# Optimization experiments

Hardware: AMD Instinct MI355X
Metric: run time of the kernel (lower is better)

The kernel has to match this reference:

```python
import jax, jax.numpy as jnp
import numpy as np

B, S, H, HD = 8, 1024, 16, 64
D = H * HD
NINF = -10000.0
EPS = 1e-6


def setup_inputs() -> dict:
    key = jax.random.key(0)
    ks = jax.random.split(key, 6)
    std = 0.02
    return {
        "x": jax.random.normal(ks[0], (B, S, D), jnp.float32),
        "mask": jax.random.randint(ks[1], (B, S), 0, 2, jnp.int32),
        "wq": jax.random.normal(ks[2], (D, D), jnp.float32) * std,
        "bq": jnp.zeros((D,), jnp.float32),
        "wk": jax.random.normal(ks[3], (D, D), jnp.float32) * std,
        "bk": jnp.zeros((D,), jnp.float32),
        "wv": jax.random.normal(ks[4], (D, D), jnp.float32) * std,
        "bv": jnp.zeros((D,), jnp.float32),
        "wo": jax.random.normal(ks[5], (D, D), jnp.float32) * std,
        "bo": jnp.zeros((D,), jnp.float32),
        "gamma": jnp.ones((D,), jnp.float32),
        "beta": jnp.zeros((D,), jnp.float32),
    }


def _heads(t):
    # [B,S,D] -> [B,H,S,HD]
    return t.reshape(t.shape[0], t.shape[1], H, HD).transpose(0, 2, 1, 3)


def _layernorm(x, gamma, beta):
    mu = jnp.mean(x, -1, keepdims=True)
    var = jnp.mean(jnp.square(x - mu), -1, keepdims=True)
    return (x - mu) * jax.lax.rsqrt(var + EPS) * gamma + beta


def reference(x, mask, wq, bq, wk, bk, wv, bv, wo, bo, gamma, beta):
    q = _heads(x @ wq + bq)
    k = _heads(x @ wk + bk)
    v = _heads(x @ wv + bv)
    scores = jnp.einsum("bhqd,bhkd->bhqk", q, k) / np.sqrt(HD).astype(np.float32)
    # padding mask broadcast over key axis: 1 = masked
    scores = scores + mask.astype(jnp.float32)[:, None, None, :] * NINF
    attn = jax.nn.softmax(scores, axis=-1)
    ctx = jnp.einsum("bhqk,bhkd->bhqd", attn, v)  # [B,H,S,HD]
    ctx = ctx.transpose(0, 2, 1, 3).reshape(B, S, D)
    out = _layernorm(x + ctx @ wo + bo, gamma, beta)
    return out
```

## Files before the change

kernel.cpp:

```cpp
#include <hip/hip_runtime.h>
#include <stdint.h>

typedef unsigned short u16;
typedef unsigned int u32;
typedef __bf16 b16x8 __attribute__((ext_vector_type(8)));
typedef float f32x4 __attribute__((ext_vector_type(4)));

#define B_ 8
#define S_ 1024
#define H_ 16
#define HD_ 64
#define D_ 1024
#define M_ 8192

__device__ __forceinline__ u16 f2bf(float f) {
  u32 u = __float_as_uint(f);
  return (u16)((u + 0x7fffu + ((u >> 16) & 1u)) >> 16);
}
__device__ __forceinline__ u16 bfbits(float f) {
  union {
    __bf16 b;
    u16 u;
  } c;
  c.b = (__bf16)f;
  return c.u;
}

__device__ __forceinline__ f32x4 mfma16(b16x8 a, b16x8 b, f32x4 c) {
  return __builtin_amdgcn_mfma_f32_16x16x32_bf16(a, b, c, 0, 0, 0);
}

__device__ __forceinline__ void cp16(const u16* g, u16* l) {
  __builtin_amdgcn_global_load_lds(
      (const __attribute__((address_space(1))) u32*)(g),
      (__attribute__((address_space(3))) u32*)(l), 16, 0, 0);
}

__global__ __launch_bounds__(1024) void wconv_kernel(
    const float* __restrict__ w0, const float* __restrict__ w1,
    const float* __restrict__ w2, const float* __restrict__ w3,
    u16* __restrict__ t0, u16* __restrict__ t1, u16* __restrict__ t2,
    u16* __restrict__ t3) {
  __shared__ float tile[32][33];
  const int z = blockIdx.z;
  const float* src = (z == 0) ? w0 : (z == 1) ? w1 : (z == 2) ? w2 : w3;
  u16* dst = (z == 0) ? t0 : (z == 1) ? t1 : (z == 2) ? t2 : t3;
  const int tx = threadIdx.x, ty = threadIdx.y;
  const int x0 = blockIdx.x * 32, y0 = blockIdx.y * 32;
  tile[ty][tx] = src[(size_t)(y0 + ty) * D_ + x0 + tx];
  __syncthreads();
  dst[(size_t)(x0 + ty) * D_ + y0 + tx] = f2bf(tile[tx][ty]);
}

__global__ __launch_bounds__(256) void xconv_kernel(const float* __restrict__ x,
                                                    u16* __restrict__ xb) {
  const size_t i = ((size_t)blockIdx.x * 256 + threadIdx.x) * 4;
  const float4 v = *(const float4*)(x + i);
  u16 o[4] = {f2bf(v.x), f2bf(v.y), f2bf(v.z), f2bf(v.w)};
  uint2 pack;
  pack.x = ((u32)o[1] << 16) | o[0];
  pack.y = ((u32)o[3] << 16) | o[2];
  *(uint2*)(xb + i) = pack;
}

#define ABUF_ 16384
#define BBUF_ 8192
#define BUFSZ_ (ABUF_ + BBUF_)

__device__ __forceinline__ void gemm256x128_mainloop(
    const u16* __restrict__ A, const u16* __restrict__ BT, int K, int m0,
    int n0, u16* lds, f32x4 (&acc)[8][2]) {
  const int t = threadIdx.x;
  const int lane = t & 63;
  const int l15 = lane & 15;
  const int q4 = lane >> 4;
  const int w = t >> 6;
  const int wm = w >> 2;
  const int wn = w & 3;

  const f32x4 zero = {0.f, 0.f, 0.f, 0.f};
#pragma unroll
  for (int mt = 0; mt < 8; ++mt)
#pragma unroll
    for (int nt = 0; nt < 2; ++nt) acc[mt][nt] = zero;

  const int rbase = t >> 3;
  const int scol = ((t & 7) ^ (rbase & 7)) * 8;
  const u16* Ag = A + (size_t)(m0 + rbase) * K + scol;
  const u16* Bg = BT + (size_t)(n0 + rbase) * K + scol;
  const int sx = l15 & 7;

  auto STAGE = [&](int kt, int bufi) {
    u16* Ab = lds + bufi * BUFSZ_;
    u16* Bb = Ab + ABUF_;
    const int k0 = kt * 64;
#pragma unroll
    for (int c = 0; c < 4; ++c)
      cp16(Ag + (size_t)(c * 64) * K + k0, Ab + c * 4096 + t * 8);
#pragma unroll
    for (int c = 0; c < 2; ++c)
      cp16(Bg + (size_t)(c * 64) * K + k0, Bb + c * 4096 + t * 8);
  };

  const int NT = K / 64;
  STAGE(0, 0);
  STAGE(1, 1);

  int cur = 0;
  for (int kt = 0; kt < NT; ++kt) {
    if (kt + 2 < NT) {
      int nb = cur + 2;
      if (nb >= 3) nb -= 3;
      STAGE(kt + 2, nb);
    }
    if (kt + 2 < NT)
      asm volatile("s_waitcnt vmcnt(12)" ::: "memory");
    else if (kt + 1 < NT)
      asm volatile("s_waitcnt vmcnt(6)" ::: "memory");
    else
      asm volatile("s_waitcnt vmcnt(0)" ::: "memory");
    asm volatile("s_barrier" ::: "memory");

    const u16* Ab = lds + cur * BUFSZ_;
    const u16* Bb = Ab + ABUF_;

    b16x8 af[8][2], bf2[2][2];
#pragma unroll
    for (int kk = 0; kk < 2; ++kk) {
      const int cc = ((kk * 4 + q4) ^ sx) * 8;
#pragma unroll
      for (int mt = 0; mt < 8; ++mt)
        af[mt][kk] = *(const b16x8*)(Ab + (wm * 128 + mt * 16 + l15) * 64 + cc);
#pragma unroll
      for (int nt = 0; nt < 2; ++nt)
        bf2[nt][kk] = *(const b16x8*)(Bb + (wn * 32 + nt * 16 + l15) * 64 + cc);
    }
    __builtin_amdgcn_sched_barrier(0);

    __builtin_amdgcn_s_setprio(1);
#pragma unroll
    for (int mt = 0; mt < 8; ++mt) {
      acc[mt][0] = mfma16(af[mt][0], bf2[0][0], acc[mt][0]);
      acc[mt][1] = mfma16(af[mt][0], bf2[1][0], acc[mt][1]);
    }
    __builtin_amdgcn_s_setprio(0);

    asm volatile("s_waitcnt lgkmcnt(0)" ::: "memory");
    asm volatile("s_barrier" ::: "memory");

    __builtin_amdgcn_s_setprio(1);
#pragma unroll
    for (int mt = 0; mt < 8; ++mt) {
      acc[mt][0] = mfma16(af[mt][1], bf2[0][1], acc[mt][0]);
      acc[mt][1] = mfma16(af[mt][1], bf2[1][1], acc[mt][1]);
    }
    __builtin_amdgcn_s_setprio(0);

    ++cur;
    if (cur == 3) cur = 0;
  }
}

__global__ __launch_bounds__(512, 2) void qkv_gemm_kernel(
    const u16* __restrict__ xb, const u16* __restrict__ wt3,
    const float* __restrict__ bq, const float* __restrict__ bk,
    const float* __restrict__ bv, u16* __restrict__ Q, u16* __restrict__ Kb,
    u16* __restrict__ VT) {
  __shared__ __align__(16) u16 lds[3 * BUFSZ_];
  const int wg = blockIdx.x;
  const int xcd = wg & 7;
  const int s = wg >> 3;
  const int by = xcd * 4 + (s & 3);
  const int bx = s >> 2;
  const int m0 = by * 256;
  const int n0 = bx * 128;

  f32x4 acc[8][2];
  gemm256x128_mainloop(xb, wt3, D_, m0, n0, lds, acc);

  const int t = threadIdx.x;
  const int lane = t & 63, w = t >> 6;
  const int l15 = lane & 15, q4 = lane >> 4;
  const int wm = w >> 2, wn = w & 3;

  const int z = n0 >> 10;
  u16* out = (z == 0) ? Q : (z == 1) ? Kb : VT;
  const float* bias = (z == 0) ? bq : (z == 1) ? bk : bv;

  for (int nt = 0; nt < 2; ++nt) {
    const int nf = n0 + wn * 32 + nt * 16 + l15;
    const int n1 = nf & 1023;
    const float bias_v = bias[n1];
    const int h = n1 >> 6, hd = n1 & 63;
    for (int mt = 0; mt < 8; ++mt) {
      for (int r = 0; r < 4; ++r) {
        const int m = m0 + wm * 128 + mt * 16 + q4 * 4 + r;
        const int b = m >> 10, ss = m & 1023;
        const float v = acc[mt][nt][r] + bias_v;
        size_t idx;
        if (z < 2)
          idx = (((size_t)(b * H_ + h)) * S_ + ss) * HD_ + hd;
        else
          idx = (((size_t)(b * H_ + h)) * HD_ + hd) * S_ + ss;
        out[idx] = f2bf(v);
      }
    }
  }
}

#define PAD_ 68
#define QPAD_ 72
__global__ __launch_bounds__(512) void attn_kernel(
    const u16* __restrict__ Q, const u16* __restrict__ Kb,
    const u16* __restrict__ VT, const int* __restrict__ mask,
    u16* __restrict__ ctx) {
  __shared__ __align__(16) u16 QPlds[128 * QPAD_];
  __shared__ __align__(16) u16 Klds[64 * PAD_];
  __shared__ __align__(16) u16 Vlds[64 * PAD_];
  __shared__ __align__(16) float Mlds[1024];

  const int t = threadIdx.x;
  const int lane = t & 63, w = t >> 6;
  const int l15 = lane & 15, q4 = lane >> 4;
  const int id = blockIdx.x;
  const int bh = id & 127;
  const int b = bh >> 4, h = bh & 15;
  const int q0 = (id >> 7) * 128;

  const u16* Qbh = Q + (size_t)bh * S_ * HD_;
  const u16* Kbh = Kb + (size_t)bh * S_ * HD_;
  const u16* Vbh = VT + (size_t)bh * S_ * HD_;
  const int* maskb = mask + b * S_;

  const int srow = t >> 3, scol = (t & 7) * 8;
  {
    b16x8 q0v = *(const b16x8*)(Qbh + (size_t)(q0 + srow) * HD_ + scol);
    b16x8 q1v = *(const b16x8*)(Qbh + (size_t)(q0 + srow + 64) * HD_ + scol);
    const int2 mv = *(const int2*)(maskb + t * 2);
    *(b16x8*)(QPlds + srow * QPAD_ + scol) = q0v;
    *(b16x8*)(QPlds + (srow + 64) * QPAD_ + scol) = q1v;
    float2 mf;
    mf.x = -14427.0f * (float)mv.x;
    mf.y = -14427.0f * (float)mv.y;
    *(float2*)(Mlds + t * 2) = mf;
  }
  __syncthreads();
  b16x8 aq[2];
  aq[0] = *(const b16x8*)(QPlds + (w * 16 + l15) * QPAD_ + q4 * 8);
  aq[1] = *(const b16x8*)(QPlds + (w * 16 + l15) * QPAD_ + 32 + q4 * 8);

  const f32x4 zero = {0.f, 0.f, 0.f, 0.f};
  f32x4 acc[4];
  for (int nt = 0; nt < 4; ++nt) acc[nt] = zero;
  float lsum = 0.f;
  u16* Pw = QPlds + w * 16 * QPAD_;
  const float c1 = 0.18033688f;

  b16x8 kv0 = *(const b16x8*)(Kbh + (size_t)srow * HD_ + scol);
  b16x8 vv0 = *(const b16x8*)(Vbh + (size_t)srow * S_ + scol);

  for (int j = 0; j < 16; ++j) {
    const int key0 = j * 64;
    __syncthreads();
    *(b16x8*)(Klds + srow * PAD_ + scol) = kv0;
    *(b16x8*)(Vlds + srow * PAD_ + scol) = vv0;
    __syncthreads();

    if (j < 15) {
      const int kn = key0 + 64;
      kv0 = *(const b16x8*)(Kbh + (size_t)(kn + srow) * HD_ + scol);
      vv0 = *(const b16x8*)(Vbh + (size_t)srow * S_ + kn + scol);
    }

    f32x4 sf[4];
    for (int nt = 0; nt < 4; ++nt) sf[nt] = zero;
    for (int kk = 0; kk < 2; ++kk)
      for (int nt = 0; nt < 4; ++nt) {
        b16x8 bk =
            *(const b16x8*)(Klds + (nt * 16 + l15) * PAD_ + kk * 32 + q4 * 8);
        sf[nt] = mfma16(bk, aq[kk], sf[nt]);
      }

    for (int nt = 0; nt < 4; ++nt) {
      const float4 mk = *(const float4*)(Mlds + key0 + nt * 16 + q4 * 4);
      float p0 = __builtin_amdgcn_exp2f(sf[nt][0] * c1 + mk.x);
      float p1 = __builtin_amdgcn_exp2f(sf[nt][1] * c1 + mk.y);
      float p2 = __builtin_amdgcn_exp2f(sf[nt][2] * c1 + mk.z);
      float p3 = __builtin_amdgcn_exp2f(sf[nt][3] * c1 + mk.w);
      lsum += (p0 + p1) + (p2 + p3);
      uint2 pk;
      pk.x = ((u32)bfbits(p1) << 16) | bfbits(p0);
      pk.y = ((u32)bfbits(p3) << 16) | bfbits(p2);
      *(uint2*)(Pw + l15 * QPAD_ + nt * 16 + q4 * 4) = pk;
    }
    asm volatile("s_waitcnt lgkmcnt(0)" ::: "memory");

    for (int kk = 0; kk < 2; ++kk) {
      b16x8 bp = *(const b16x8*)(Pw + l15 * QPAD_ + kk * 32 + q4 * 8);
      for (int nt = 0; nt < 4; ++nt) {
        b16x8 vb =
            *(const b16x8*)(Vlds + (nt * 16 + l15) * PAD_ + kk * 32 + q4 * 8);
        acc[nt] = mfma16(vb, bp, acc[nt]);
      }
    }
  }

  lsum += __shfl_xor(lsum, 16);
  lsum += __shfl_xor(lsum, 32);
  const float inv = 1.0f / lsum;

  const int srw = q0 + w * 16 + l15;
  u16* crow = ctx + ((size_t)(b * S_ + srw)) * D_ + h * 64;
  for (int nt = 0; nt < 4; ++nt) {
    uint2 pk;
    pk.x = ((u32)bfbits(acc[nt][1] * inv) << 16) | bfbits(acc[nt][0] * inv);
    pk.y = ((u32)bfbits(acc[nt][3] * inv) << 16) | bfbits(acc[nt][2] * inv);
    *(uint2*)(crow + nt * 16 + q4 * 4) = pk;
  }
}

__global__ __launch_bounds__(512, 2) void out_gemm_kernel(
    const u16* __restrict__ ctx, const u16* __restrict__ wto,
    const float* __restrict__ bo, const float* __restrict__ x,
    float* __restrict__ y) {
  __shared__ __align__(16) u16 lds[3 * BUFSZ_];
  const int wg = blockIdx.x;
  const int xcd = wg & 7;
  const int s = wg >> 3;
  const int by = xcd * 4 + (s & 3);
  const int bx = s >> 2;
  const int m0 = by * 256, n0 = bx * 128;

  f32x4 acc[8][2];
  gemm256x128_mainloop(ctx, wto, D_, m0, n0, lds, acc);

  const int t = threadIdx.x;
  const int lane = t & 63, w = t >> 6;
  const int l15 = lane & 15, q4 = lane >> 4;
  const int wm = w >> 2, wn = w & 3;

  for (int nt = 0; nt < 2; ++nt) {
    const int n = n0 + wn * 32 + nt * 16 + l15;
    const float bias = bo[n];
    for (int mt = 0; mt < 8; ++mt) {
      for (int r = 0; r < 4; ++r) {
        const int m = m0 + wm * 128 + mt * 16 + q4 * 4 + r;
        y[(size_t)m * D_ + n] = acc[mt][nt][r] + bias + x[(size_t)m * D_ + n];
      }
    }
  }
}

__global__ __launch_bounds__(256) void ln_kernel(const float* __restrict__ y,
                                                 const float* __restrict__ g,
                                                 const float* __restrict__ be,
                                                 float* __restrict__ out) {
  const int row = blockIdx.x, t = threadIdx.x;
  const float* yr = y + (size_t)row * D_;
  const float4 v = *(const float4*)(yr + t * 4);
  float s = v.x + v.y + v.z + v.w;
  float ss = v.x * v.x + v.y * v.y + v.z * v.z + v.w * v.w;
  for (int off = 1; off < 64; off <<= 1) {
    s += __shfl_xor(s, off);
    ss += __shfl_xor(ss, off);
  }
  __shared__ float red[8];
  const int w = t >> 6, lane = t & 63;
  if (lane == 0) {
    red[w] = s;
    red[4 + w] = ss;
  }
  __syncthreads();
  s = red[0] + red[1] + red[2] + red[3];
  ss = red[4] + red[5] + red[6] + red[7];
  const float mu = s * (1.f / 1024.f);
  const float var = ss * (1.f / 1024.f) - mu * mu;
  const float rs = rsqrtf(var + 1e-6f);
  const int c = t * 4;
  const float4 gv = *(const float4*)(g + c);
  const float4 bv = *(const float4*)(be + c);
  float4 o;
  o.x = (v.x - mu) * rs * gv.x + bv.x;
  o.y = (v.y - mu) * rs * gv.y + bv.y;
  o.z = (v.z - mu) * rs * gv.z + bv.z;
  o.w = (v.w - mu) * rs * gv.w + bv.w;
  *(float4*)(out + (size_t)row * D_ + c) = o;
}

extern "C" void kernel_launch(void* const* d_in, const int* in_sizes, int n_in,
                              void* d_out, int out_size, void* d_ws,
                              size_t ws_size, hipStream_t stream) {
  const float* x = (const float*)d_in[0];
  const int* mask = (const int*)d_in[1];
  const float* wq = (const float*)d_in[2];
  const float* bq = (const float*)d_in[3];
  const float* wk = (const float*)d_in[4];
  const float* bk = (const float*)d_in[5];
  const float* wv = (const float*)d_in[6];
  const float* bv = (const float*)d_in[7];
  const float* wo = (const float*)d_in[8];
  const float* bo = (const float*)d_in[9];
  const float* gamma = (const float*)d_in[10];
  const float* beta = (const float*)d_in[11];
  float* out = (float*)d_out;

  char* ws = (char*)d_ws;
  const size_t MB = 1024ull * 1024ull;
  u16* wtq = (u16*)(ws + 0 * MB);
  u16* wtk = (u16*)(ws + 2 * MB);
  u16* wtv = (u16*)(ws + 4 * MB);
  u16* wto = (u16*)(ws + 6 * MB);
  u16* xb = (u16*)(ws + 8 * MB);
  u16* ctx = (u16*)(ws + 8 * MB);
  u16* Qb = (u16*)(ws + 24 * MB);
  u16* Kb = (u16*)(ws + 40 * MB);
  u16* VTb = (u16*)(ws + 56 * MB);
  float* y = (float*)(ws + 24 * MB);

  wconv_kernel<<<dim3(32, 32, 4), dim3(32, 32), 0, stream>>>(
      wq, wk, wv, wo, wtq, wtk, wtv, wto);
  xconv_kernel<<<8192, 256, 0, stream>>>(x, xb);
  qkv_gemm_kernel<<<768, 512, 0, stream>>>(xb, wtq, bq, bk, bv, Qb, Kb, VTb);
  attn_kernel<<<1024, 512, 0, stream>>>(Qb, Kb, VTb, mask, ctx);
  out_gemm_kernel<<<256, 512, 0, stream>>>(ctx, wto, bo, x, y);
  ln_kernel<<<8192, 256, 0, stream>>>(y, gamma, beta, out);
}
```

Before: 285.3 us.

## Rewrite QKV GEMM with 256x256 tiles and fine-grained interleaved double-buffer pipeline

The QKV projection GEMM moves from 256x128 tiles with a 3-stage buffer to 256x256 tiles with two LDS buffers of 64 KB each, halving the grid to 384 workgroups. The K loop is hand-unrolled into sub-steps that interleave A and B tile prefetches with LDS fragment loads and MFMA bursts, separated by barriers and sched_barriers. The larger tile raises data reuse per global load. In exchange it uses more accumulator registers and LDS, which may cut occupancy and leave fewer workgroups than CUs, and it adds many barriers.

Result: slower. 364.4 us (+27.7%).

```diff
diff --git a/kernel.cpp b/kernel.cpp
--- a/kernel.cpp
+++ b/kernel.cpp
@@ -63,132 +63,220 @@
   *(uint2*)(xb + i) = pack;
 }
 
-#define ABUF_ 16384
-#define BBUF_ 8192
-#define BUFSZ_ (ABUF_ + BBUF_)
-
-__device__ __forceinline__ void gemm256x128_mainloop(
-    const u16* __restrict__ A, const u16* __restrict__ BT, int K, int m0,
-    int n0, u16* lds, f32x4 (&acc)[8][2]) {
-  const int t = threadIdx.x;
-  const int lane = t & 63;
-  const int l15 = lane & 15;
-  const int q4 = lane >> 4;
-  const int w = t >> 6;
-  const int wm = w >> 2;
-  const int wn = w & 3;
-
-  const f32x4 zero = {0.f, 0.f, 0.f, 0.f};
-#pragma unroll
-  for (int mt = 0; mt < 8; ++mt)
-#pragma unroll
-    for (int nt = 0; nt < 2; ++nt) acc[mt][nt] = zero;
-
-  const int rbase = t >> 3;
-  const int scol = ((t & 7) ^ (rbase & 7)) * 8;
-  const u16* Ag = A + (size_t)(m0 + rbase) * K + scol;
-  const u16* Bg = BT + (size_t)(n0 + rbase) * K + scol;
-  const int sx = l15 & 7;
-
-  auto STAGE = [&](int kt, int bufi) {
-    u16* Ab = lds + bufi * BUFSZ_;
-    u16* Bb = Ab + ABUF_;
-    const int k0 = kt * 64;
-#pragma unroll
-    for (int c = 0; c < 4; ++c)
-      cp16(Ag + (size_t)(c * 64) * K + k0, Ab + c * 4096 + t * 8);
-#pragma unroll
-    for (int c = 0; c < 2; ++c)
-      cp16(Bg + (size_t)(c * 64) * K + k0, Bb + c * 4096 + t * 8);
-  };
-
-  const int NT = K / 64;
-  STAGE(0, 0);
-  STAGE(1, 1);
-
-  int cur = 0;
-  for (int kt = 0; kt < NT; ++kt) {
-    if (kt + 2 < NT) {
-      int nb = cur + 2;
-      if (nb >= 3) nb -= 3;
-      STAGE(kt + 2, nb);
-    }
-    if (kt + 2 < NT)
-      asm volatile("s_waitcnt vmcnt(12)" ::: "memory");
-    else if (kt + 1 < NT)
-      asm volatile("s_waitcnt vmcnt(6)" ::: "memory");
-    else
-      asm volatile("s_waitcnt vmcnt(0)" ::: "memory");
-    asm volatile("s_barrier" ::: "memory");
-
-    const u16* Ab = lds + cur * BUFSZ_;
-    const u16* Bb = Ab + ABUF_;
-
-    b16x8 af[8][2], bf2[2][2];
-#pragma unroll
-    for (int kk = 0; kk < 2; ++kk) {
-      const int cc = ((kk * 4 + q4) ^ sx) * 8;
-#pragma unroll
-      for (int mt = 0; mt < 8; ++mt)
-        af[mt][kk] = *(const b16x8*)(Ab + (wm * 128 + mt * 16 + l15) * 64 + cc);
-#pragma unroll
-      for (int nt = 0; nt < 2; ++nt)
-        bf2[nt][kk] = *(const b16x8*)(Bb + (wn * 32 + nt * 16 + l15) * 64 + cc);
-    }
-    __builtin_amdgcn_sched_barrier(0);
-
-    __builtin_amdgcn_s_setprio(1);
-#pragma unroll
-    for (int mt = 0; mt < 8; ++mt) {
-      acc[mt][0] = mfma16(af[mt][0], bf2[0][0], acc[mt][0]);
-      acc[mt][1] = mfma16(af[mt][0], bf2[1][0], acc[mt][1]);
-    }
-    __builtin_amdgcn_s_setprio(0);
-
-    asm volatile("s_waitcnt lgkmcnt(0)" ::: "memory");
-    asm volatile("s_barrier" ::: "memory");
-
-    __builtin_amdgcn_s_setprio(1);
-#pragma unroll
-    for (int mt = 0; mt < 8; ++mt) {
-      acc[mt][0] = mfma16(af[mt][1], bf2[0][1], acc[mt][0]);
-      acc[mt][1] = mfma16(af[mt][1], bf2[1][1], acc[mt][1]);
-    }
-    __builtin_amdgcn_s_setprio(0);
-
-    ++cur;
-    if (cur == 3) cur = 0;
-  }
-}
-
 __global__ __launch_bounds__(512, 2) void qkv_gemm_kernel(
     const u16* __restrict__ xb, const u16* __restrict__ wt3,
     const float* __restrict__ bq, const float* __restrict__ bk,
     const float* __restrict__ bv, u16* __restrict__ Q, u16* __restrict__ Kb,
     u16* __restrict__ VT) {
-  __shared__ __align__(16) u16 lds[3 * BUFSZ_];
+  __shared__ __align__(16) u16 lds[65536];
   const int wg = blockIdx.x;
   const int xcd = wg & 7;
   const int s = wg >> 3;
   const int by = xcd * 4 + (s & 3);
   const int bx = s >> 2;
   const int m0 = by * 256;
-  const int n0 = bx * 128;
-
-  f32x4 acc[8][2];
-  gemm256x128_mainloop(xb, wt3, D_, m0, n0, lds, acc);
+  const int n0 = bx * 256;
 
   const int t = threadIdx.x;
   const int lane = t & 63, w = t >> 6;
   const int l15 = lane & 15, q4 = lane >> 4;
   const int wm = w >> 2, wn = w & 3;
 
+  const int rbase = t >> 3;
+  const int scol = ((t & 7) ^ (rbase & 7)) * 8;
+  const u16* Ag = xb + (size_t)(m0 + rbase) * D_ + scol;
+  const u16* Bg = wt3 + (size_t)(n0 + rbase) * D_ + scol;
+
+  auto STAGE_A = [&](int kt) {
+    u16* dst = lds + (kt & 1) * 32768;
+    const int k0 = kt * 64;
+#pragma unroll
+    for (int c = 0; c < 4; ++c)
+      cp16(Ag + (size_t)(c * 64) * D_ + k0, dst + c * 4096 + t * 8);
+  };
+  auto STAGE_B = [&](int kt) {
+    u16* dst = lds + (kt & 1) * 32768 + 16384;
+    const int k0 = kt * 64;
+#pragma unroll
+    for (int c = 0; c < 4; ++c)
+      cp16(Bg + (size_t)(c * 64) * D_ + k0, dst + c * 4096 + t * 8);
+  };
+
+  const f32x4 zero = {0.f, 0.f, 0.f, 0.f};
+  f32x4 acc[8][4];
+#pragma unroll
+  for (int mf = 0; mf < 8; ++mf)
+#pragma unroll
+    for (int nc = 0; nc < 4; ++nc) acc[mf][nc] = zero;
+
+  const int sx = l15 & 7;
+  const int abase = wm * 8192 + l15 * 64;
+  const int bbase = 16384 + wn * 4096 + l15 * 64;
+  const int cc0 = (q4 ^ sx) * 8;
+  const int cc1 = ((4 + q4) ^ sx) * 8;
+
+  STAGE_A(0);
+  STAGE_B(0);
+  STAGE_A(1);
+
+#pragma unroll 1
+  for (int i = 0; i < 8; ++i) {
+    const int kt0 = 2 * i, kt1 = 2 * i + 1;
+    const u16* be_ = lds;
+    const u16* bo_ = lds + 32768;
+    const bool pf = (i < 7);
+    b16x8 af[8], bfa, bfb;
+
+    asm volatile("s_waitcnt vmcnt(4)" ::: "memory");
+    asm volatile("s_barrier" ::: "memory");
+#pragma unroll
+    for (int mf = 0; mf < 8; ++mf)
+      af[mf] = *(const b16x8*)(be_ + abase + mf * 1024 + cc0);
+    bfa = *(const b16x8*)(be_ + bbase + cc0);
+    bfb = *(const b16x8*)(be_ + bbase + 1024 + cc0);
+    STAGE_B(kt1);
+    asm volatile("s_barrier" ::: "memory");
+    asm volatile("s_waitcnt lgkmcnt(0)" ::: "memory");
+    __builtin_amdgcn_sched_barrier(0);
+    __builtin_amdgcn_s_setprio(1);
+#pragma unroll
+    for (int mf = 0; mf < 8; ++mf) {
+      acc[mf][0] = mfma16(af[mf], bfa, acc[mf][0]);
+      acc[mf][1] = mfma16(af[mf], bfb, acc[mf][1]);
+    }
+    __builtin_amdgcn_s_setprio(0);
+    asm volatile("s_barrier" ::: "memory");
+    __builtin_amdgcn_sched_barrier(0);
+
+    bfa = *(const b16x8*)(be_ + bbase + 2048 + cc0);
+    bfb = *(const b16x8*)(be_ + bbase + 3072 + cc0);
+    asm volatile("s_barrier" ::: "memory");
+    asm volatile("s_waitcnt lgkmcnt(0)" ::: "memory");
+    __builtin_amdgcn_sched_barrier(0);
+    __builtin_amdgcn_s_setprio(1);
+#pragma unroll
+    for (int mf = 0; mf < 8; ++mf) {
+      acc[mf][2] = mfma16(af[mf], bfa, acc[mf][2]);
+      acc[mf][3] = mfma16(af[mf], bfb, acc[mf][3]);
+    }
+    __builtin_amdgcn_s_setprio(0);
+    asm volatile("s_barrier" ::: "memory");
+    __builtin_amdgcn_sched_barrier(0);
+
+#pragma unroll
+    for (int mf = 0; mf < 8; ++mf)
+      af[mf] = *(const b16x8*)(be_ + abase + mf * 1024 + cc1);
+    bfa = *(const b16x8*)(be_ + bbase + cc1);
+    bfb = *(const b16x8*)(be_ + bbase + 1024 + cc1);
+    asm volatile("s_barrier" ::: "memory");
+    asm volatile("s_waitcnt lgkmcnt(0)" ::: "memory");
+    __builtin_amdgcn_sched_barrier(0);
+    __builtin_amdgcn_s_setprio(1);
+#pragma unroll
+    for (int mf = 0; mf < 8; ++mf) {
+      acc[mf][0] = mfma16(af[mf], bfa, acc[mf][0]);
+      acc[mf][1] = mfma16(af[mf], bfb, acc[mf][1]);
+    }
+    __builtin_amdgcn_s_setprio(0);
+    asm volatile("s_barrier" ::: "memory");
+    __builtin_amdgcn_sched_barrier(0);
+
+    bfa = *(const b16x8*)(be_ + bbase + 2048 + cc1);
+    bfb = *(const b16x8*)(be_ + bbase + 3072 + cc1);
+    if (pf) STAGE_A(kt0 + 2);
+    asm volatile("s_barrier" ::: "memory");
+    asm volatile("s_waitcnt lgkmcnt(0)" ::: "memory");
+    __builtin_amdgcn_sched_barrier(0);
+    __builtin_amdgcn_s_setprio(1);
+#pragma unroll
+    for (int mf = 0; mf < 8; ++mf) {
+      acc[mf][2] = mfma16(af[mf], bfa, acc[mf][2]);
+      acc[mf][3] = mfma16(af[mf], bfb, acc[mf][3]);
+    }
+    __builtin_amdgcn_s_setprio(0);
+    asm volatile("s_barrier" ::: "memory");
+    __builtin_amdgcn_sched_barrier(0);
+
+    if (pf)
+      asm volatile("s_waitcnt vmcnt(4)" ::: "memory");
+    else
+      asm volatile("s_waitcnt vmcnt(0)" ::: "memory");
+    asm volatile("s_barrier" ::: "memory");
+#pragma unroll
+    for (int mf = 0; mf < 8; ++mf)
+      af[mf] = *(const b16x8*)(bo_ + abase + mf * 1024 + cc0);
+    bfa = *(const b16x8*)(bo_ + bbase + cc0);
+    bfb = *(const b16x8*)(bo_ + bbase + 1024 + cc0);
+    if (pf) STAGE_B(kt0 + 2);
+    asm volatile("s_barrier" ::: "memory");
+    asm volatile("s_waitcnt lgkmcnt(0)" ::: "memory");
+    __builtin_amdgcn_sched_barrier(0);
+    __builtin_amdgcn_s_setprio(1);
+#pragma unroll
+    for (int mf = 0; mf < 8; ++mf) {
+      acc[mf][0] = mfma16(af[mf], bfa, acc[mf][0]);
+      acc[mf][1] = mfma16(af[mf], bfb, acc[mf][1]);
+    }
+    __builtin_amdgcn_s_setprio(0);
+    asm volatile("s_barrier" ::: "memory");
+    __builtin_amdgcn_sched_barrier(0);
+
+    bfa = *(const b16x8*)(bo_ + bbase + 2048 + cc0);
+    bfb = *(const b16x8*)(bo_ + bbase + 3072 + cc0);
+    asm volatile("s_barrier" ::: "memory");
+    asm volatile("s_waitcnt lgkmcnt(0)" ::: "memory");
+    __builtin_amdgcn_sched_barrier(0);
+    __builtin_amdgcn_s_setprio(1);
+#pragma unroll
+    for (int mf = 0; mf < 8; ++mf) {
+      acc[mf][2] = mfma16(af[mf], bfa, acc[mf][2]);
+      acc[mf][3] = mfma16(af[mf], bfb, acc[mf][3]);
+    }
+    __builtin_amdgcn_s_setprio(0);
+    asm volatile("s_barrier" ::: "memory");
+    __builtin_amdgcn_sched_barrier(0);
+
+#pragma unroll
+    for (int mf = 0; mf < 8; ++mf)
+      af[mf] = *(const b16x8*)(bo_ + abase + mf * 1024 + cc1);
+    bfa = *(const b16x8*)(bo_ + bbase + cc1);
+    bfb = *(const b16x8*)(bo_ + bbase + 1024 + cc1);
+    asm volatile("s_barrier" ::: "memory");
+    asm volatile("s_waitcnt lgkmcnt(0)" ::: "memory");
+    __builtin_amdgcn_sched_barrier(0);
+    __builtin_amdgcn_s_setprio(1);
+#pragma unroll
+    for (int mf = 0; mf < 8; ++mf) {
+      acc[mf][0] = mfma16(af[mf], bfa, acc[mf][0]);
+      acc[mf][1] = mfma16(af[mf], bfb, acc[mf][1]);
+    }
+    __builtin_amdgcn_s_setprio(0);
+    asm volatile("s_barrier" ::: "memory");
+    __builtin_amdgcn_sched_barrier(0);
+
+    bfa = *(const b16x8*)(bo_ + bbase + 2048 + cc1);
+    bfb = *(const b16x8*)(bo_ + bbase + 3072 + cc1);
+    if (pf) STAGE_A(kt1 + 2);
+    asm volatile("s_barrier" ::: "memory");
+    asm volatile("s_waitcnt lgkmcnt(0)" ::: "memory");
+    __builtin_amdgcn_sched_barrier(0);
+    __builtin_amdgcn_s_setprio(1);
+#pragma unroll
+    for (int mf = 0; mf < 8; ++mf) {
+      acc[mf][2] = mfma16(af[mf], bfa, acc[mf][2]);
+      acc[mf][3] = mfma16(af[mf], bfb, acc[mf][3]);
+    }
+    __builtin_amdgcn_s_setprio(0);
+    asm volatile("s_barrier" ::: "memory");
+    __builtin_amdgcn_sched_barrier(0);
+  }
+
   const int z = n0 >> 10;
   u16* out = (z == 0) ? Q : (z == 1) ? Kb : VT;
   const float* bias = (z == 0) ? bq : (z == 1) ? bk : bv;
 
-  for (int nt = 0; nt < 2; ++nt) {
-    const int nf = n0 + wn * 32 + nt * 16 + l15;
+  for (int nt = 0; nt < 4; ++nt) {
+    const int nf = n0 + wn * 64 + nt * 16 + l15;
     const int n1 = nf & 1023;
     const float bias_v = bias[n1];
     const int h = n1 >> 6, hd = n1 & 63;
@@ -205,6 +293,104 @@
         out[idx] = f2bf(v);
       }
     }
+  }
+}
+
+#define ABUF_ 16384
+#define BBUF_ 8192
+#define BUFSZ_ (ABUF_ + BBUF_)
+
+__device__ __forceinline__ void gemm256x128_mainloop(
+    const u16* __restrict__ A, const u16* __restrict__ BT, int K, int m0,
+    int n0, u16* lds, f32x4 (&acc)[8][2]) {
+  const int t = threadIdx.x;
+  const int lane = t & 63;
+  const int l15 = lane & 15;
+  const int q4 = lane >> 4;
+  const int w = t >> 6;
+  const int wm = w >> 2;
+  const int wn = w & 3;
+
+  const f32x4 zero = {0.f, 0.f, 0.f, 0.f};
+#pragma unroll
+  for (int mt = 0; mt < 8; ++mt)
+#pragma unroll
+    for (int nt = 0; nt < 2; ++nt) acc[mt][nt] = zero;
+
+  const int rbase = t >> 3;
+  const int scol = ((t & 7) ^ (rbase & 7)) * 8;
+  const u16* Ag = A + (size_t)(m0 + rbase) * K + scol;
+  const u16* Bg = BT + (size_t)(n0 + rbase) * K + scol;
+  const int sx = l15 & 7;
+
+  auto STAGE = [&](int kt, int bufi) {
+    u16* Ab = lds + bufi * BUFSZ_;
+    u16* Bb = Ab + ABUF_;
+    const int k0 = kt * 64;
+#pragma unroll
+    for (int c = 0; c < 4; ++c)
+      cp16(Ag + (size_t)(c * 64) * K + k0, Ab + c * 4096 + t * 8);
+#pragma unroll
+    for (int c = 0; c < 2; ++c)
+      cp16(Bg + (size_t)(c * 64) * K + k0, Bb + c * 4096 + t * 8);
+  };
+
+  const int NT = K / 64;
+  STAGE(0, 0);
+  STAGE(1, 1);
+
+  int cur = 0;
+  for (int kt = 0; kt < NT; ++kt) {
+    if (kt + 2 < NT) {
+      int nb = cur + 2;
+      if (nb >= 3) nb -= 3;
+      STAGE(kt + 2, nb);
+    }
+    if (kt + 2 < NT)
+      asm volatile("s_waitcnt vmcnt(12)" ::: "memory");
+    else if (kt + 1 < NT)
+      asm volatile("s_waitcnt vmcnt(6)" ::: "memory");
+    else
+      asm volatile("s_waitcnt vmcnt(0)" ::: "memory");
+    asm volatile("s_barrier" ::: "memory");
+
+    const u16* Ab = lds + cur * BUFSZ_;
+    const u16* Bb = Ab + ABUF_;
+
+    b16x8 af[8][2], bf2[2][2];
+#pragma unroll
+    for (int kk = 0; kk < 2; ++kk) {
+      const int cc = ((kk * 4 + q4) ^ sx) * 8;
+#pragma unroll
+      for (int mt = 0; mt < 8; ++mt)
+        af[mt][kk] = *(const b16x8*)(Ab + (wm * 128 + mt * 16 + l15) * 64 + cc);
+#pragma unroll
+      for (int nt = 0; nt < 2; ++nt)
+        bf2[nt][kk] = *(const b16x8*)(Bb + (wn * 32 + nt * 16 + l15) * 64 + cc);
+    }
+    __builtin_amdgcn_sched_barrier(0);
+
+    __builtin_amdgcn_s_setprio(1);
+#pragma unroll
+    for (int mt = 0; mt < 8; ++mt) {
+      acc[mt][0] = mfma16(af[mt][0], bf2[0][0], acc[mt][0]);
+      acc[mt][1] = mfma16(af[mt][0], bf2[1][0], acc[mt][1]);
+    }
+    __builtin_amdgcn_s_setprio(0);
+
+    asm volatile("s_waitcnt lgkmcnt(0)" ::: "memory");
+    asm volatile("s_barrier" ::: "memory");
+
+    __builtin_amdgcn_s_setprio(1);
+#pragma unroll
+    for (int mt = 0; mt < 8; ++mt) {
+      acc[mt][0] = mfma16(af[mt][1], bf2[0][1], acc[mt][0]);
+      acc[mt][1] = mfma16(af[mt][1], bf2[1][1], acc[mt][1]);
+    }
+    __builtin_amdgcn_s_setprio(0);
+
+    ++cur;
+    if (cur == 3) cur = 0;
   }
 }
 
@@ -420,7 +606,7 @@
   wconv_kernel<<<dim3(32, 32, 4), dim3(32, 32), 0, stream>>>(
       wq, wk, wv, wo, wtq, wtk, wtv, wto);
   xconv_kernel<<<8192, 256, 0, stream>>>(x, xb);
-  qkv_gemm_kernel<<<768, 512, 0, stream>>>(xb, wtq, bq, bk, bv, Qb, Kb, VTb);
+  qkv_gemm_kernel<<<384, 512, 0, stream>>>(xb, wtq, bq, bk, bv, Qb, Kb, VTb);
   attn_kernel<<<1024, 512, 0, stream>>>(Qb, Kb, VTb, mask, ctx);
   out_gemm_kernel<<<256, 512, 0, stream>>>(ctx, wto, bo, x, y);
   ln_kernel<<<8192, 256, 0, stream>>>(y, gamma, beta, out);
```
